# Optimization experiments

Measured on AMD Instinct MI355X. Metric: run time of the kernel, lower is better.

The kernel has to match this reference:

```python
import jax, jax.numpy as jnp
import numpy as np

EMB = 768
HEADS = 12
HEAD_DIM = EMB // HEADS


def setup_inputs() -> dict:
    key = jax.random.key(0)
    ks = jax.random.split(key, 9)
    B, L, D = 4, 2048, EMB
    s = 1.0 / np.sqrt(D)
    return {
        "x": jax.random.normal(ks[0], (B, L, D), dtype=jnp.float32),
        "Wq": jax.random.normal(ks[1], (D, D), dtype=jnp.float32) * s,
        "bq": jnp.zeros((D,), dtype=jnp.float32),
        "Wk": jax.random.normal(ks[2], (D, D), dtype=jnp.float32) * s,
        "bk": jnp.zeros((D,), dtype=jnp.float32),
        "Wv": jax.random.normal(ks[3], (D, D), dtype=jnp.float32) * s,
        "bv": jnp.zeros((D,), dtype=jnp.float32),
        "Wo": jax.random.normal(ks[4], (D, D), dtype=jnp.float32) * s,
        "bo": jnp.zeros((D,), dtype=jnp.float32),
    }


def reference(x, Wq, bq, Wk, bk, Wv, bv, Wo, bo):
    B, L, D = x.shape
    H, hd = HEADS, HEAD_DIM
    # QKV projections -> [B, H, L, hd]
    def proj(W, b):
        return (x @ W + b).reshape(B, L, H, hd).transpose(0, 2, 1, 3)
    Q = proj(Wq, bq)
    K = proj(Wk, bk)
    V = proj(Wv, bv)
    # scores [B, H, L, L]
    scores = jnp.einsum("bhqd,bhkd->bhqk", Q, K) / jnp.sqrt(jnp.float32(hd))
    attn = jax.nn.softmax(scores, axis=-1)
    out = jnp.einsum("bhqk,bhkd->bhqd", attn, V)  # [B,H,L,hd]
    out = out.transpose(0, 2, 1, 3).reshape(B, L, D)
    return out @ Wo + bo
```

## Files before the change

kernel.cpp:

```cpp
#include <hip/hip_runtime.h>
#include <math.h>

#define TL 2048
#define TD 768
#define NH 12
#define HD 64
#define NB 4
#define MTOT (NB * TL)

typedef __bf16 bf16;
typedef __attribute__((ext_vector_type(4))) __bf16 bf16x4;
typedef __attribute__((ext_vector_type(8))) __bf16 bf16x8;
typedef __attribute__((ext_vector_type(4))) float floatx4;

#define QSCALE 0.18033688011112042f

#define MFMA16(A, B, C) __builtin_amdgcn_mfma_f32_16x16x32_bf16(A, B, C, 0, 0, 0)

__device__ __forceinline__ void gl_lds16(const void* g, void* l) {
    __builtin_amdgcn_global_load_lds(
        (const __attribute__((address_space(1))) void*)g,
        (__attribute__((address_space(3))) void*)l, 16, 0, 0);
}

__device__ __forceinline__ floatx4 exp2x4(floatx4 a) {
    floatx4 r;
    r.x = __builtin_amdgcn_exp2f(a.x);
    r.y = __builtin_amdgcn_exp2f(a.y);
    r.z = __builtin_amdgcn_exp2f(a.z);
    r.w = __builtin_amdgcn_exp2f(a.w);
    return r;
}

__device__ __forceinline__ int kperm_inv(int r) {
    return (r & 35) | (((r >> 2) & 3) << 3) | (((r >> 4) & 1) << 2);
}

__global__ __launch_bounds__(256)
void prep_kernel(const float* __restrict__ x,
                 const float* __restrict__ W0, const float* __restrict__ W1,
                 const float* __restrict__ W2, const float* __restrict__ W3,
                 bf16* __restrict__ xb,
                 bf16* __restrict__ T0, bf16* __restrict__ T1,
                 bf16* __restrict__ T2, bf16* __restrict__ T3)
{
    __shared__ float Ts[64][65];
    const int bid = blockIdx.x;
    const int t = threadIdx.x;
    if (bid < 576) {
        const int z = bid / 144, rem = bid % 144;
        const float* W = z == 0 ? W0 : z == 1 ? W1 : z == 2 ? W2 : W3;
        bf16*       T = z == 0 ? T0 : z == 1 ? T1 : z == 2 ? T2 : T3;
        const int k0 = (rem / 12) * 64, n0 = (rem % 12) * 64;
        const int rr = t >> 4, cc = (t & 15) * 4;
#pragma unroll
        for (int i = 0; i < 4; ++i) {
            int row = rr + i * 16;
            float4 v = *(const float4*)(W + (size_t)(k0 + row) * TD + n0 + cc);
            Ts[row][cc] = v.x; Ts[row][cc + 1] = v.y;
            Ts[row][cc + 2] = v.z; Ts[row][cc + 3] = v.w;
        }
        __syncthreads();
#pragma unroll
        for (int i = 0; i < 4; ++i) {
            int n = rr + i * 16;
            bf16x4 pk;
#pragma unroll
            for (int j = 0; j < 4; ++j) pk[j] = (bf16)Ts[cc + j][n];
            *(bf16x4*)(T + (size_t)(n0 + n) * TD + k0 + cc) = pk;
        }
    } else {
        size_t i = ((size_t)(bid - 576) * 256 + t) * 4;
        float4 v = *(const float4*)(x + i);
        bf16x4 o;
        o[0] = (bf16)v.x; o[1] = (bf16)v.y; o[2] = (bf16)v.z; o[3] = (bf16)v.w;
        *(bf16x4*)(xb + i) = o;
    }
}

__global__ __launch_bounds__(256)
void qkv_gemm(const bf16* __restrict__ xb,
              const bf16* __restrict__ Wqt, const bf16* __restrict__ Wkt,
              const bf16* __restrict__ Wvt,
              const float* __restrict__ bq, const float* __restrict__ bk,
              const float* __restrict__ bv,
              bf16* __restrict__ Q, bf16* __restrict__ K, bf16* __restrict__ Vt)
{
    __shared__ __align__(16) bf16 As[128 * 64];
    __shared__ __align__(16) bf16 Bs[128 * 64];
    __shared__ __align__(16) bf16 Eb[4][16 * 72];

    const int t = threadIdx.x;
    const int lane = t & 63, w = t >> 6;
    const int quad = lane >> 4, l16 = lane & 15;
    const int m0 = blockIdx.x * 128;
    const int n0 = blockIdx.y * 128;
    const int which = blockIdx.z;
    const bf16*  W    = which == 0 ? Wqt : which == 1 ? Wkt : Wvt;
    const float* bias = which == 0 ? bq  : which == 1 ? bk  : bv;
    const float scale = which == 0 ? QSCALE : 1.0f;

    const int rm = (w >> 1) * 64, cn = (w & 1) * 64;

    floatx4 acc[4][4];
#pragma unroll
    for (int i = 0; i < 4; ++i)
#pragma unroll
        for (int j = 0; j < 4; ++j) acc[i][j] = (floatx4){0.f, 0.f, 0.f, 0.f};

    const bf16* gA[4];
    const bf16* gB[4];
#pragma unroll
    for (int i = 0; i < 4; ++i) {
        int n = t + i * 256, r = n >> 3, s = ((n & 7) ^ (r & 7)) * 8;
        gA[i] = xb + (size_t)(m0 + r) * TD + s;
        gB[i] = W + (size_t)(n0 + r) * TD + s;
    }

    for (int kk = 0; kk < TD; kk += 64) {
#pragma unroll
        for (int i = 0; i < 4; ++i) {
            gl_lds16(gA[i] + kk, As + t * 8 + i * 2048);
            gl_lds16(gB[i] + kk, Bs + t * 8 + i * 2048);
        }
        __syncthreads();
#pragma unroll
        for (int ks = 0; ks < 2; ++ks) {
            bf16x8 af[4], bfr[4];
#pragma unroll
            for (int mb = 0; mb < 4; ++mb) {
                int r = rm + mb * 16 + l16;
                af[mb] = *(const bf16x8*)&As[r * 64 + (((ks * 4 + quad) ^ (r & 7)) * 8)];
            }
#pragma unroll
            for (int nb = 0; nb < 4; ++nb) {
                int r = cn + nb * 16 + l16;
                bfr[nb] = *(const bf16x8*)&Bs[r * 64 + (((ks * 4 + quad) ^ (r & 7)) * 8)];
            }
#pragma unroll
            for (int mb = 0; mb < 4; ++mb)
#pragma unroll
                for (int nb = 0; nb < 4; ++nb)
                    acc[mb][nb] = MFMA16(af[mb], bfr[nb], acc[mb][nb]);
        }
        __syncthreads();
    }

    float bsc[4];
#pragma unroll
    for (int nb = 0; nb < 4; ++nb)
        bsc[nb] = bias[n0 + cn + nb * 16 + l16] * scale;

    const int token0 = m0 + rm;
    const int b  = token0 >> 11;
    const int l0 = token0 & (TL - 1);
    const int h  = (n0 + cn) >> 6;
    const int bh = b * NH + h;
    bf16* Ew = Eb[w];

    if (which < 2) {
        bf16* gp = (which == 0 ? Q : K) + ((size_t)bh * TL + l0) * HD;
#pragma unroll
        for (int mb = 0; mb < 4; ++mb) {
#pragma unroll
            for (int nb = 0; nb < 4; ++nb)
#pragma unroll
                for (int r = 0; r < 4; ++r)
                    Ew[(quad * 4 + r) * 72 + nb * 16 + l16] =
                        (bf16)(acc[mb][nb][r] * scale + bsc[nb]);
#pragma unroll
            for (int i = 0; i < 2; ++i) {
                int row = i * 8 + (lane >> 3), seg = lane & 7;
                bf16x8 v = *(const bf16x8*)&Ew[row * 72 + seg * 8];
                *(bf16x8*)(gp + (size_t)(mb * 16 + row) * HD + seg * 8) = v;
            }
        }
    } else {
#pragma unroll
        for (int nb = 0; nb < 4; ++nb) {
#pragma unroll
            for (int mb = 0; mb < 4; ++mb) {
                bf16x4 pk;
#pragma unroll
                for (int r = 0; r < 4; ++r) pk[r] = (bf16)(acc[mb][nb][r] + bsc[nb]);
                *(bf16x4*)&Ew[l16 * 72 + mb * 16 + quad * 4] = pk;
            }
#pragma unroll
            for (int i = 0; i < 2; ++i) {
                int row = i * 8 + (lane >> 3), seg = lane & 7;
                bf16x8 v = *(const bf16x8*)&Ew[row * 72 + seg * 8];
                *(bf16x8*)(Vt + ((size_t)bh * HD + nb * 16 + row) * TL + l0 + seg * 8) = v;
            }
        }
    }
}

__global__ __launch_bounds__(256)
void attn_kernel(const bf16* __restrict__ Q, const bf16* __restrict__ K,
                 const bf16* __restrict__ Vt, bf16* __restrict__ O)
{
    __shared__ __align__(16) bf16 Ks[2][64 * 64];
    __shared__ __align__(16) bf16 Vs[2][64 * 64];

    const int t = threadIdx.x;
    const int lane = t & 63, w = t >> 6;
    const int quad = lane >> 4, l16 = lane & 15;

    const int n = blockIdx.y * gridDim.x + blockIdx.x;
    const int xcd = n & 7, s = n >> 3;
    const int bh = xcd * 6 + (s >> 4);
    const int q0 = (s & 15) * 128;

    const bf16* Qb = Q + (size_t)bh * TL * HD;
    const bf16* Kb = K + (size_t)bh * TL * HD;
    const bf16* Vb = Vt + (size_t)bh * HD * TL;

    const int qw = q0 + w * 32;
    bf16x8 qf[2][2];
#pragma unroll
    for (int mb = 0; mb < 2; ++mb)
#pragma unroll
        for (int ks = 0; ks < 2; ++ks)
            qf[mb][ks] = *(const bf16x8*)(Qb + (size_t)(qw + mb * 16 + l16) * HD
                                          + ks * 32 + quad * 8);

    float lrow[2] = {0.f, 0.f};
    floatx4 o[2][4];
#pragma unroll
    for (int mb = 0; mb < 2; ++mb)
#pragma unroll
        for (int db = 0; db < 4; ++db) o[mb][db] = (floatx4){0.f, 0.f, 0.f, 0.f};

    const bf16* gK[2];
    const bf16* gV[2];
#pragma unroll
    for (int i = 0; i < 2; ++i) {
        int nn = t + i * 256, r = nn >> 3, sg = ((nn & 7) ^ (r & 7)) * 8;
        gK[i] = Kb + (size_t)kperm_inv(r) * HD + sg;
        gV[i] = Vb + (size_t)r * TL + sg;
    }

#pragma unroll
    for (int i = 0; i < 2; ++i) {
        gl_lds16(gK[i], Ks[0] + t * 8 + i * 2048);
        gl_lds16(gV[i], Vs[0] + t * 8 + i * 2048);
    }

    for (int kt = 0; kt < TL / 64; ++kt) {
        const int cur = kt & 1;
        __syncthreads();
        if (kt + 1 < TL / 64) {
            const int k1 = (kt + 1) * 64;
#pragma unroll
            for (int i = 0; i < 2; ++i) {
                gl_lds16(gK[i] + (size_t)k1 * HD, Ks[cur ^ 1] + t * 8 + i * 2048);
                gl_lds16(gV[i] + k1,              Vs[cur ^ 1] + t * 8 + i * 2048);
            }
        }
        const bf16* Kc = Ks[cur];
        const bf16* Vc = Vs[cur];

        floatx4 s2[2][4];
#pragma unroll
        for (int nb = 0; nb < 4; ++nb) {
            int r = nb * 16 + l16;
            bf16x8 kf0 = *(const bf16x8*)&Kc[r * 64 + ((quad ^ (r & 7)) * 8)];
            bf16x8 kf1 = *(const bf16x8*)&Kc[r * 64 + (((4 + quad) ^ (r & 7)) * 8)];
#pragma unroll
            for (int mb = 0; mb < 2; ++mb) {
                floatx4 a = (floatx4){0.f, 0.f, 0.f, 0.f};
                a = MFMA16(kf0, qf[mb][0], a);
                a = MFMA16(kf1, qf[mb][1], a);
                s2[mb][nb] = a;
            }
        }

        bf16x8 pA[2][2];
#pragma unroll
        for (int mb = 0; mb < 2; ++mb) {
#pragma unroll
            for (int ks = 0; ks < 2; ++ks) {
                floatx4 p0 = exp2x4(s2[mb][2 * ks]);
                floatx4 p1 = exp2x4(s2[mb][2 * ks + 1]);
                lrow[mb] += (p0.x + p0.y + p0.z + p0.w) + (p1.x + p1.y + p1.z + p1.w);
                bf16x8 pk;
                pk[0] = (bf16)p0.x; pk[1] = (bf16)p0.y; pk[2] = (bf16)p0.z; pk[3] = (bf16)p0.w;
                pk[4] = (bf16)p1.x; pk[5] = (bf16)p1.y; pk[6] = (bf16)p1.z; pk[7] = (bf16)p1.w;
                pA[mb][ks] = pk;
            }
        }

#pragma unroll
        for (int ks = 0; ks < 2; ++ks) {
#pragma unroll
            for (int db = 0; db < 4; ++db) {
                int r = db * 16 + l16;
                bf16x8 vf = *(const bf16x8*)&Vc[r * 64 + (((ks * 4 + quad) ^ (r & 7)) * 8)];
#pragma unroll
                for (int mb = 0; mb < 2; ++mb)
                    o[mb][db] = MFMA16(pA[mb][ks], vf, o[mb][db]);
            }
        }
    }

    const int b = bh / NH, h = bh % NH;
#pragma unroll
    for (int mb = 0; mb < 2; ++mb) {
        lrow[mb] += __shfl_xor(lrow[mb], 16);
        lrow[mb] += __shfl_xor(lrow[mb], 32);
        floatx4 inv;
#pragma unroll
        for (int r = 0; r < 4; ++r)
            inv[r] = 1.0f / __shfl(lrow[mb], (lane & 48) | (quad * 4 + r));
#pragma unroll
        for (int db = 0; db < 4; ++db)
#pragma unroll
            for (int r = 0; r < 4; ++r) {
                int l = qw + mb * 16 + quad * 4 + r;
                O[((size_t)b * TL + l) * TD + h * HD + db * 16 + l16] =
                    (bf16)(o[mb][db][r] * inv[r]);
            }
    }
}

__global__ __launch_bounds__(256)
void oproj_gemm(const bf16* __restrict__ A, const bf16* __restrict__ Wt,
                const float* __restrict__ bo, float* __restrict__ out)
{
    __shared__ __align__(16) bf16 As[128 * 64];
    __shared__ __align__(16) bf16 Bs[128 * 64];
    __shared__ __align__(16) float Ef[4][16 * 68];

    const int t = threadIdx.x;
    const int lane = t & 63, w = t >> 6;
    const int quad = lane >> 4, l16 = lane & 15;
    const int m0 = blockIdx.x * 128;
    const int n0 = blockIdx.y * 128;
    const int rm = (w >> 1) * 64, cn = (w & 1) * 64;

    floatx4 acc[4][4];
#pragma unroll
    for (int i = 0; i < 4; ++i)
#pragma unroll
        for (int j = 0; j < 4; ++j) acc[i][j] = (floatx4){0.f, 0.f, 0.f, 0.f};

    const bf16* gA[4];
    const bf16* gB[4];
#pragma unroll
    for (int i = 0; i < 4; ++i) {
        int n = t + i * 256, r = n >> 3, s = ((n & 7) ^ (r & 7)) * 8;
        gA[i] = A + (size_t)(m0 + r) * TD + s;
        gB[i] = Wt + (size_t)(n0 + r) * TD + s;
    }

    for (int kk = 0; kk < TD; kk += 64) {
#pragma unroll
        for (int i = 0; i < 4; ++i) {
            gl_lds16(gA[i] + kk, As + t * 8 + i * 2048);
            gl_lds16(gB[i] + kk, Bs + t * 8 + i * 2048);
        }
        __syncthreads();
#pragma unroll
        for (int ks = 0; ks < 2; ++ks) {
            bf16x8 af[4], bfr[4];
#pragma unroll
            for (int mb = 0; mb < 4; ++mb) {
                int r = rm + mb * 16 + l16;
                af[mb] = *(const bf16x8*)&As[r * 64 + (((ks * 4 + quad) ^ (r & 7)) * 8)];
            }
#pragma unroll
            for (int nb = 0; nb < 4; ++nb) {
                int r = cn + nb * 16 + l16;
                bfr[nb] = *(const bf16x8*)&Bs[r * 64 + (((ks * 4 + quad) ^ (r & 7)) * 8)];
            }
#pragma unroll
            for (int mb = 0; mb < 4; ++mb)
#pragma unroll
                for (int nb = 0; nb < 4; ++nb)
                    acc[mb][nb] = MFMA16(af[mb], bfr[nb], acc[mb][nb]);
        }
        __syncthreads();
    }

    float bb[4];
#pragma unroll
    for (int nb = 0; nb < 4; ++nb) bb[nb] = bo[n0 + cn + nb * 16 + l16];

    float* Ew = Ef[w];
#pragma unroll
    for (int mb = 0; mb < 4; ++mb) {
#pragma unroll
        for (int nb = 0; nb < 4; ++nb)
#pragma unroll
            for (int r = 0; r < 4; ++r)
                Ew[(quad * 4 + r) * 68 + nb * 16 + l16] = acc[mb][nb][r] + bb[nb];
#pragma unroll
        for (int i = 0; i < 4; ++i) {
            int row = i * 4 + (lane >> 4), seg = lane & 15;
            float4 v = *(const float4*)&Ew[row * 68 + seg * 4];
            *(float4*)(out + (size_t)(m0 + rm + mb * 16 + row) * TD + n0 + cn + seg * 4) = v;
        }
    }
}

extern "C" void kernel_launch(void* const* d_in, const int* in_sizes, int n_in,
                              void* d_out, int out_size, void* d_ws, size_t ws_size,
                              hipStream_t stream)
{
    const float* x  = (const float*)d_in[0];
    const float* Wq = (const float*)d_in[1];
    const float* bq = (const float*)d_in[2];
    const float* Wk = (const float*)d_in[3];
    const float* bk = (const float*)d_in[4];
    const float* Wv = (const float*)d_in[5];
    const float* bv = (const float*)d_in[6];
    const float* Wo = (const float*)d_in[7];
    const float* bo = (const float*)d_in[8];

    const size_t NXE = (size_t)MTOT * TD;
    const size_t NWE = (size_t)TD * TD;

    bf16* xb  = (bf16*)d_ws;
    bf16* Wqt = xb + NXE;
    bf16* Wkt = Wqt + NWE;
    bf16* Wvt = Wkt + NWE;
    bf16* Wot = Wvt + NWE;
    bf16* Qb  = Wot + NWE;
    bf16* Kb  = Qb + NXE;
    bf16* Vtb = Kb + NXE;
    bf16* Ob  = Vtb + NXE;

    prep_kernel<<<576 + 6144, 256, 0, stream>>>(x, Wq, Wk, Wv, Wo,
                                                xb, Wqt, Wkt, Wvt, Wot);
    qkv_gemm<<<dim3(MTOT / 128, TD / 128, 3), 256, 0, stream>>>(
        xb, Wqt, Wkt, Wvt, bq, bk, bv, Qb, Kb, Vtb);
    attn_kernel<<<dim3(TL / 128, NB * NH), 256, 0, stream>>>(Qb, Kb, Vtb, Ob);
    oproj_gemm<<<dim3(MTOT / 128, TD / 128), 256, 0, stream>>>(Ob, Wot, bo,
                                                               (float*)d_out);
}
```

Before: 218.0 us.

## Restructure attention to 2 waves with 64 rows each, shrink oproj N tile

The attention kernel drops from 4 waves of 32 query rows to 2 waves of 64 rows per block. This doubles the register reuse of each K/V fragment loaded from LDS, but it removes the double-buffered prefetch, so each tile load now sits between two barriers. The S computation is also split per k-step to limit register pressure. Separately, the output projection tile shrinks from 128x128 to 128x64, doubling the number of blocks for better occupancy and tail balance.

```diff
diff --git a/kernel.cpp b/kernel.cpp
--- a/kernel.cpp
+++ b/kernel.cpp
@@ -195,12 +195,12 @@
     }
 }
 
-__global__ __launch_bounds__(256)
+__global__ __launch_bounds__(128)
 void attn_kernel(const bf16* __restrict__ Q, const bf16* __restrict__ K,
                  const bf16* __restrict__ Vt, bf16* __restrict__ O)
 {
-    __shared__ __align__(16) bf16 Ks[2][64 * 64];
-    __shared__ __align__(16) bf16 Vs[2][64 * 64];
+    __shared__ __align__(16) bf16 Ks[64 * 64];
+    __shared__ __align__(16) bf16 Vs[64 * 64];
 
     const int t = threadIdx.x;
     const int lane = t & 63, w = t >> 6;
@@ -215,73 +215,62 @@
     const bf16* Kb = K + (size_t)bh * TL * HD;
     const bf16* Vb = Vt + (size_t)bh * HD * TL;
 
-    const int qw = q0 + w * 32;
-    bf16x8 qf[2][2];
-#pragma unroll
-    for (int mb = 0; mb < 2; ++mb)
+    const int qw = q0 + w * 64;
+    bf16x8 qf[4][2];
+#pragma unroll
+    for (int mb = 0; mb < 4; ++mb)
 #pragma unroll
         for (int ks = 0; ks < 2; ++ks)
             qf[mb][ks] = *(const bf16x8*)(Qb + (size_t)(qw + mb * 16 + l16) * HD
                                           + ks * 32 + quad * 8);
 
-    float lrow[2] = {0.f, 0.f};
-    floatx4 o[2][4];
-#pragma unroll
-    for (int mb = 0; mb < 2; ++mb)
+    float lrow[4] = {0.f, 0.f, 0.f, 0.f};
+    floatx4 o[4][4];
+#pragma unroll
+    for (int mb = 0; mb < 4; ++mb)
 #pragma unroll
         for (int db = 0; db < 4; ++db) o[mb][db] = (floatx4){0.f, 0.f, 0.f, 0.f};
 
-    const bf16* gK[2];
-    const bf16* gV[2];
-#pragma unroll
-    for (int i = 0; i < 2; ++i) {
-        int nn = t + i * 256, r = nn >> 3, sg = ((nn & 7) ^ (r & 7)) * 8;
+    const bf16* gK[4];
+    const bf16* gV[4];
+#pragma unroll
+    for (int i = 0; i < 4; ++i) {
+        int nn = t + i * 128, r = nn >> 3, sg = ((nn & 7) ^ (r & 7)) * 8;
         gK[i] = Kb + (size_t)kperm_inv(r) * HD + sg;
         gV[i] = Vb + (size_t)r * TL + sg;
     }
 
-#pragma unroll
-    for (int i = 0; i < 2; ++i) {
-        gl_lds16(gK[i], Ks[0] + t * 8 + i * 2048);
-        gl_lds16(gV[i], Vs[0] + t * 8 + i * 2048);
-    }
-
     for (int kt = 0; kt < TL / 64; ++kt) {
-        const int cur = kt & 1;
-        __syncthreads();
-        if (kt + 1 < TL / 64) {
-            const int k1 = (kt + 1) * 64;
-#pragma unroll
-            for (int i = 0; i < 2; ++i) {
-                gl_lds16(gK[i] + (size_t)k1 * HD, Ks[cur ^ 1] + t * 8 + i * 2048);
-                gl_lds16(gV[i] + k1,              Vs[cur ^ 1] + t * 8 + i * 2048);
-            }
-        }
-        const bf16* Kc = Ks[cur];
-        const bf16* Vc = Vs[cur];
-
-        floatx4 s2[2][4];
-#pragma unroll
-        for (int nb = 0; nb < 4; ++nb) {
-            int r = nb * 16 + l16;
-            bf16x8 kf0 = *(const bf16x8*)&Kc[r * 64 + ((quad ^ (r & 7)) * 8)];
-            bf16x8 kf1 = *(const bf16x8*)&Kc[r * 64 + (((4 + quad) ^ (r & 7)) * 8)];
-#pragma unroll
-            for (int mb = 0; mb < 2; ++mb) {
-                floatx4 a = (floatx4){0.f, 0.f, 0.f, 0.f};
-                a = MFMA16(kf0, qf[mb][0], a);
-                a = MFMA16(kf1, qf[mb][1], a);
-                s2[mb][nb] = a;
-            }
-        }
-
-        bf16x8 pA[2][2];
-#pragma unroll
-        for (int mb = 0; mb < 2; ++mb) {
-#pragma unroll
-            for (int ks = 0; ks < 2; ++ks) {
-                floatx4 p0 = exp2x4(s2[mb][2 * ks]);
-                floatx4 p1 = exp2x4(s2[mb][2 * ks + 1]);
+        const int k0 = kt * 64;
+        __syncthreads();
+#pragma unroll
+        for (int i = 0; i < 4; ++i) {
+            gl_lds16(gK[i] + (size_t)k0 * HD, Ks + (t + i * 128) * 8);
+            gl_lds16(gV[i] + k0,              Vs + (t + i * 128) * 8);
+        }
+        __syncthreads();
+
+        bf16x8 pA[4][2];
+#pragma unroll
+        for (int ks = 0; ks < 2; ++ks) {
+            floatx4 s2[4][2];
+#pragma unroll
+            for (int nbp = 0; nbp < 2; ++nbp) {
+                int rr = (ks * 2 + nbp) * 16 + l16;
+                bf16x8 kf0 = *(const bf16x8*)&Ks[rr * 64 + ((quad ^ (rr & 7)) * 8)];
+                bf16x8 kf1 = *(const bf16x8*)&Ks[rr * 64 + (((4 + quad) ^ (rr & 7)) * 8)];
+#pragma unroll
+                for (int mb = 0; mb < 4; ++mb) {
+                    floatx4 a = (floatx4){0.f, 0.f, 0.f, 0.f};
+                    a = MFMA16(kf0, qf[mb][0], a);
+                    a = MFMA16(kf1, qf[mb][1], a);
+                    s2[mb][nbp] = a;
+                }
+            }
+#pragma unroll
+            for (int mb = 0; mb < 4; ++mb) {
+                floatx4 p0 = exp2x4(s2[mb][0]);
+                floatx4 p1 = exp2x4(s2[mb][1]);
                 lrow[mb] += (p0.x + p0.y + p0.z + p0.w) + (p1.x + p1.y + p1.z + p1.w);
                 bf16x8 pk;
                 pk[0] = (bf16)p0.x; pk[1] = (bf16)p0.y; pk[2] = (bf16)p0.z; pk[3] = (bf16)p0.w;
@@ -294,10 +283,10 @@
         for (int ks = 0; ks < 2; ++ks) {
 #pragma unroll
             for (int db = 0; db < 4; ++db) {
-                int r = db * 16 + l16;
-                bf16x8 vf = *(const bf16x8*)&Vc[r * 64 + (((ks * 4 + quad) ^ (r & 7)) * 8)];
-#pragma unroll
-                for (int mb = 0; mb < 2; ++mb)
+                int rr = db * 16 + l16;
+                bf16x8 vf = *(const bf16x8*)&Vs[rr * 64 + (((ks * 4 + quad) ^ (rr & 7)) * 8)];
+#pragma unroll
+                for (int mb = 0; mb < 4; ++mb)
                     o[mb][db] = MFMA16(pA[mb][ks], vf, o[mb][db]);
             }
         }
@@ -305,7 +294,7 @@
 
     const int b = bh / NH, h = bh % NH;
 #pragma unroll
-    for (int mb = 0; mb < 2; ++mb) {
+    for (int mb = 0; mb < 4; ++mb) {
         lrow[mb] += __shfl_xor(lrow[mb], 16);
         lrow[mb] += __shfl_xor(lrow[mb], 32);
         floatx4 inv;
@@ -328,76 +317,81 @@
                 const float* __restrict__ bo, float* __restrict__ out)
 {
     __shared__ __align__(16) bf16 As[128 * 64];
-    __shared__ __align__(16) bf16 Bs[128 * 64];
-    __shared__ __align__(16) float Ef[4][16 * 68];
+    __shared__ __align__(16) bf16 Bs[64 * 64];
+    __shared__ __align__(16) float Ef[4][16 * 36];
 
     const int t = threadIdx.x;
     const int lane = t & 63, w = t >> 6;
     const int quad = lane >> 4, l16 = lane & 15;
     const int m0 = blockIdx.x * 128;
-    const int n0 = blockIdx.y * 128;
-    const int rm = (w >> 1) * 64, cn = (w & 1) * 64;
-
-    floatx4 acc[4][4];
+    const int n0 = blockIdx.y * 64;
+    const int rm = (w >> 1) * 64, cn = (w & 1) * 32;
+
+    floatx4 acc[4][2];
 #pragma unroll
     for (int i = 0; i < 4; ++i)
 #pragma unroll
-        for (int j = 0; j < 4; ++j) acc[i][j] = (floatx4){0.f, 0.f, 0.f, 0.f};
+        for (int j = 0; j < 2; ++j) acc[i][j] = (floatx4){0.f, 0.f, 0.f, 0.f};
 
     const bf16* gA[4];
-    const bf16* gB[4];
+    const bf16* gB[2];
 #pragma unroll
     for (int i = 0; i < 4; ++i) {
-        int n = t + i * 256, r = n >> 3, s = ((n & 7) ^ (r & 7)) * 8;
+        int nn = t + i * 256, r = nn >> 3, s = ((nn & 7) ^ (r & 7)) * 8;
         gA[i] = A + (size_t)(m0 + r) * TD + s;
+    }
+#pragma unroll
+    for (int i = 0; i < 2; ++i) {
+        int nn = t + i * 256, r = nn >> 3, s = ((nn & 7) ^ (r & 7)) * 8;
         gB[i] = Wt + (size_t)(n0 + r) * TD + s;
     }
 
     for (int kk = 0; kk < TD; kk += 64) {
 #pragma unroll
-        for (int i = 0; i < 4; ++i) {
-            gl_lds16(gA[i] + kk, As + t * 8 + i * 2048);
-            gl_lds16(gB[i] + kk, Bs + t * 8 + i * 2048);
-        }
+        for (int i = 0; i < 4; ++i)
+            gl_lds16(gA[i] + kk, As + (t + i * 256) * 8);
+#pragma unroll
+        for (int i = 0; i < 2; ++i)
+            gl_lds16(gB[i] + kk, Bs + (t + i * 256) * 8);
         __syncthreads();
 #pragma unroll
         for (int ks = 0; ks < 2; ++ks) {
-            bf16x8 af[4], bfr[4];
+            bf16x8 af[4], bfr[2];
 #pragma unroll
             for (int mb = 0; mb < 4; ++mb) {
                 int r = rm + mb * 16 + l16;
                 af[mb] = *(const bf16x8*)&As[r * 64 + (((ks * 4 + quad) ^ (r & 7)) * 8)];
             }
 #pragma unroll
-            for (int nb = 0; nb < 4; ++nb) {
+            for (int nb = 0; nb < 2; ++nb) {
                 int r = cn + nb * 16 + l16;
                 bfr[nb] = *(const bf16x8*)&Bs[r * 64 + (((ks * 4 + quad) ^ (r & 7)) * 8)];
             }
 #pragma unroll
             for (int mb = 0; mb < 4; ++mb)
 #pragma unroll
-                for (int nb = 0; nb < 4; ++nb)
+                for (int nb = 0; nb < 2; ++nb)
                     acc[mb][nb] = MFMA16(af[mb], bfr[nb], acc[mb][nb]);
         }
         __syncthreads();
     }
 
-    float bb[4];
-#pragma unroll
-    for (int nb = 0; nb < 4; ++nb) bb[nb] = bo[n0 + cn + nb * 16 + l16];
+    float bb[2];
+#pragma unroll
+    for (int nb = 0; nb < 2; ++nb) bb[nb] = bo[n0 + cn + nb * 16 + l16];
 
     float* Ew = Ef[w];
 #pragma unroll
     for (int mb = 0; mb < 4; ++mb) {
 #pragma unroll
-        for (int nb = 0; nb < 4; ++nb)
+        for (int nb = 0; nb < 2; ++nb)
 #pragma unroll
             for (int r = 0; r < 4; ++r)
-                Ew[(quad * 4 + r) * 68 + nb * 16 + l16] = acc[mb][nb][r] + bb[nb];
-#pragma unroll
-        for (int i = 0; i < 4; ++i) {
-            int row = i * 4 + (lane >> 4), seg = lane & 15;
-            float4 v = *(const float4*)&Ew[row * 68 + seg * 4];
+                Ew[(quad * 4 + r) * 36 + nb * 16 + l16] = acc[mb][nb][r] + bb[nb];
+#pragma unroll
+        for (int i = 0; i < 2; ++i) {
+            int row = i * 8 + (lane >> 3), seg = lane & 7;
+            float4 v = *(const float4*)&Ew[row * 36 + seg * 4];
             *(float4*)(out + (size_t)(m0 + rm + mb * 16 + row) * TD + n0 + cn + seg * 4) = v;
         }
     }
@@ -434,7 +428,7 @@
                                                 xb, Wqt, Wkt, Wvt, Wot);
     qkv_gemm<<<dim3(MTOT / 128, TD / 128, 3), 256, 0, stream>>>(
         xb, Wqt, Wkt, Wvt, bq, bk, bv, Qb, Kb, Vtb);
-    attn_kernel<<<dim3(TL / 128, NB * NH), 256, 0, stream>>>(Qb, Kb, Vtb, Ob);
-    oproj_gemm<<<dim3(MTOT / 128, TD / 128), 256, 0, stream>>>(Ob, Wot, bo,
-                                                               (float*)d_out);
-}
+    attn_kernel<<<dim3(TL / 128, NB * NH), 128, 0, stream>>>(Qb, Kb, Vtb, Ob);
+    oproj_gemm<<<dim3(MTOT / 128, TD / 64), 256, 0, stream>>>(Ob, Wot, bo,
+                                                              (float*)d_out);
+}
```

After: 258.6 us. +18.6%, slower.
